# Performance work log

Hardware: AMD Instinct MI355X
Metric: run time of the kernel (lower is better)

## Reference

```python
import jax, jax.numpy as jnp
import numpy as np

B, L, D = 2, 4096, 128      # batch, seq_len, d_model
ED = 2 * D                  # d_inner (expand=2) = 256
N = 16                      # d_state
K = 4                       # d_conv
R = (D + 15) // 16          # dt_rank = 8
H = 2 * D                   # mlp hidden = 256


def setup_inputs() -> dict:
    key = jax.random.key(0)
    ks = jax.random.split(key, 20)
    s = 0.05
    inp = {
        "x": jax.random.normal(ks[0], (B, L, D), dtype=jnp.float32),
        # outer block LayerNorm (norm1)
        "norm1_g": jnp.ones((D,), jnp.float32),
        "norm1_b": jnp.zeros((D,), jnp.float32),
        # MambaLayer inner LayerNorm
        "inner_g": jnp.ones((D,), jnp.float32),
        "inner_b": jnp.zeros((D,), jnp.float32),
        # Mamba params
        "in_w": jax.random.normal(ks[1], (2 * ED, D), jnp.float32) * s,      # in_proj (no bias)
        "conv_w": jax.random.normal(ks[2], (ED, 1, K), jnp.float32) * s,     # depthwise conv
        "conv_b": jax.random.normal(ks[3], (ED,), jnp.float32) * s,
        "xproj_w": jax.random.normal(ks[4], (R + 2 * N, ED), jnp.float32) * s,  # x_proj (no bias)
        "dt_w": jax.random.normal(ks[5], (ED, R), jnp.float32) * s,
        "dt_b": jax.random.normal(ks[6], (ED,), jnp.float32) * s,
        "A_log": jnp.tile(jnp.log(jnp.arange(1, N + 1, dtype=jnp.float32)), (ED, 1)),  # [ED,N]
        "Dp": jnp.ones((ED,), jnp.float32),
        "out_w": jax.random.normal(ks[7], (D, ED), jnp.float32) * s,         # out_proj (no bias)
        # MLP
        "fc1_w": jax.random.normal(ks[8], (H, D), jnp.float32) * s,
        "fc1_b": jnp.zeros((H,), jnp.float32),
        "fc2_w": jax.random.normal(ks[9], (D, H), jnp.float32) * s,
        "fc2_b": jnp.zeros((D,), jnp.float32),
    }
    return inp


def _ln(x, g, b, eps=1e-5):
    m = jnp.mean(x, axis=-1, keepdims=True)
    v = jnp.mean((x - m) ** 2, axis=-1, keepdims=True)
    return (x - m) * jax.lax.rsqrt(v + eps) * g + b


def _mamba(x, in_w, conv_w, conv_b, xproj_w, dt_w, dt_b, A_log, Dp, out_w):
    # x: [B, L, D]
    xz = jnp.einsum('bld,ed->ble', x, in_w)          # [B,L,2*ED]
    u, z = jnp.split(xz, 2, axis=-1)                 # each [B,L,ED]
    # causal depthwise conv1d over L
    u_c = jnp.transpose(u, (0, 2, 1))                # [B,ED,L]
    u_c = jax.lax.conv_general_dilated(
        u_c, conv_w, window_strides=(1,), padding=[(K - 1, 0)],
        dimension_numbers=('NCH', 'OIH', 'NCH'), feature_group_count=ED)
    u = jax.nn.silu(jnp.transpose(u_c, (0, 2, 1)) + conv_b)   # [B,L,ED]
    # input-dependent dt, B, C
    dbc = jnp.einsum('ble,re->blr', u, xproj_w)      # [B,L,R+2N]
    dt, Bm, Cm = jnp.split(dbc, [R, R + N], axis=-1)
    delta = jax.nn.softplus(jnp.einsum('blr,er->ble', dt, dt_w) + dt_b)  # [B,L,ED]
    A = -jnp.exp(A_log)                              # [ED,N]
    deltaA = jnp.exp(jnp.einsum('ble,en->blen', delta, A))               # [B,L,ED,N]
    deltaBu = jnp.einsum('ble,bln,ble->blen', delta, Bm, u)              # [B,L,ED,N]
    # selective scan over L
    def step(h, inp):
        dA, dBu, Ct = inp                            # [B,ED,N],[B,ED,N],[B,N]
        h = dA * h + dBu
        y = jnp.einsum('ben,bn->be', h, Ct)
        return h, y
    h0 = jnp.zeros((B, ED, N), u.dtype)
    xs = (jnp.transpose(deltaA, (1, 0, 2, 3)),
          jnp.transpose(deltaBu, (1, 0, 2, 3)),
          jnp.transpose(Cm, (1, 0, 2)))
    _, ys = jax.lax.scan(step, h0, xs)               # [L,B,ED]
    y = jnp.transpose(ys, (1, 0, 2)) + u * Dp        # [B,L,ED]
    y = y * jax.nn.silu(z)
    return jnp.einsum('ble,de->bld', y, out_w)       # [B,L,D]


def reference(x, norm1_g, norm1_b, inner_g, inner_b, in_w, conv_w, conv_b,
              xproj_w, dt_w, dt_b, A_log, Dp, out_w, fc1_w, fc1_b, fc2_w, fc2_b):
    # attn branch: mamba(inner_LN(norm1(x)))
    a = _mamba(_ln(_ln(x, norm1_g, norm1_b), inner_g, inner_b),
               in_w, conv_w, conv_b, xproj_w, dt_w, dt_b, A_log, Dp, out_w)
    x = x + a
    # mlp branch (note: original applies norm1 again to updated x)
    h = _ln(x, norm1_g, norm1_b)
    h = jax.nn.gelu(jnp.einsum('bld,hd->blh', h, fc1_w) + fc1_b, approximate=False)
    h = jnp.einsum('blh,dh->bld', h, fc2_w) + fc2_b
    return x + h
```

## Files before the change

### kernel.cpp

```cpp
#include <hip/hip_runtime.h>
#include <hip/hip_bf16.h>
#include <math.h>

#define BB 2
#define LL 4096
#define DD 128
#define ED 256
#define NN 16
#define KK 4
#define RR 8
#define HH 256
#define NT (BB*LL)
#define NC 128
#define LC 32

#define LOG2E 1.4426950408889634f

typedef __attribute__((ext_vector_type(8))) short short8;
typedef __attribute__((ext_vector_type(8))) unsigned short ushort8v;
typedef __attribute__((ext_vector_type(4))) float floatx4;

__device__ __forceinline__ unsigned short f2bf(float f) {
  unsigned int b = __builtin_bit_cast(unsigned int, f);
  b += 0x7FFFu + ((b >> 16) & 1u);
  return (unsigned short)(b >> 16);
}

__device__ __forceinline__ float exp2_fast(float x) {
#if __has_builtin(__builtin_amdgcn_exp2f)
  return __builtin_amdgcn_exp2f(x);
#else
  return exp2f(x);
#endif
}

__device__ __forceinline__ ushort8v pack8(const float4& v0, const float4& v1) {
  ushort8v p;
  p[0]=f2bf(v0.x); p[1]=f2bf(v0.y); p[2]=f2bf(v0.z); p[3]=f2bf(v0.w);
  p[4]=f2bf(v1.x); p[5]=f2bf(v1.y); p[6]=f2bf(v1.z); p[7]=f2bf(v1.w);
  return p;
}

__global__ __launch_bounds__(256) void gemm_inln_k(const float* __restrict__ x,
    const float* __restrict__ g1, const float* __restrict__ b1,
    const float* __restrict__ g2, const float* __restrict__ b2,
    const float* __restrict__ W, float* __restrict__ C) {
  __shared__ unsigned short As[64][136];
  __shared__ unsigned short Ws[64][136];
  const int row0 = blockIdx.y * 64;
  const int col0 = blockIdx.x * 64;
  const int tid  = threadIdx.x;
  const int wave = tid >> 6, lane = tid & 63;
  const int quad = lane >> 4, l16 = lane & 15;
  const int wm = (wave & 1) * 32, wn = (wave >> 1) * 32;
  const int lr = tid >> 2;
  const int lk = (tid & 3) * 32;

  {
    const float* Ap = x + (size_t)(row0 + lr)*DD + lk;
    float4 av[8];
    float s = 0.f, sq = 0.f;
    #pragma unroll
    for (int g = 0; g < 8; g++) {
      av[g] = *(const float4*)(Ap + g*4);
      s  += av[g].x + av[g].y + av[g].z + av[g].w;
      sq += av[g].x*av[g].x + av[g].y*av[g].y + av[g].z*av[g].z + av[g].w*av[g].w;
    }
    s += __shfl_xor(s, 1);  s += __shfl_xor(s, 2);
    sq += __shfl_xor(sq, 1); sq += __shfl_xor(sq, 2);
    const float m1 = s * (1.f/128.f);
    const float rs1 = rsqrtf(sq*(1.f/128.f) - m1*m1 + 1e-5f);
    float s2 = 0.f, sq2 = 0.f;
    #pragma unroll
    for (int g = 0; g < 8; g++) {
      const float4 gg = *(const float4*)(g1 + lk + g*4);
      const float4 bb = *(const float4*)(b1 + lk + g*4);
      av[g].x = (av[g].x - m1)*rs1*gg.x + bb.x;
      av[g].y = (av[g].y - m1)*rs1*gg.y + bb.y;
      av[g].z = (av[g].z - m1)*rs1*gg.z + bb.z;
      av[g].w = (av[g].w - m1)*rs1*gg.w + bb.w;
      s2  += av[g].x + av[g].y + av[g].z + av[g].w;
      sq2 += av[g].x*av[g].x + av[g].y*av[g].y + av[g].z*av[g].z + av[g].w*av[g].w;
    }
    s2 += __shfl_xor(s2, 1);  s2 += __shfl_xor(s2, 2);
    sq2 += __shfl_xor(sq2, 1); sq2 += __shfl_xor(sq2, 2);
    const float m2 = s2 * (1.f/128.f);
    const float rs2 = rsqrtf(sq2*(1.f/128.f) - m2*m2 + 1e-5f);
    #pragma unroll
    for (int g = 0; g < 4; g++) {
      const float4 ga = *(const float4*)(g2 + lk + g*8);
      const float4 gb = *(const float4*)(g2 + lk + g*8 + 4);
      const float4 ba = *(const float4*)(b2 + lk + g*8);
      const float4 bbv= *(const float4*)(b2 + lk + g*8 + 4);
      ushort8v pa;
      pa[0] = f2bf((av[2*g].x   - m2)*rs2*ga.x + ba.x);
      pa[1] = f2bf((av[2*g].y   - m2)*rs2*ga.y + ba.y);
      pa[2] = f2bf((av[2*g].z   - m2)*rs2*ga.z + ba.z);
      pa[3] = f2bf((av[2*g].w   - m2)*rs2*ga.w + ba.w);
      pa[4] = f2bf((av[2*g+1].x - m2)*rs2*gb.x + bbv.x);
      pa[5] = f2bf((av[2*g+1].y - m2)*rs2*gb.y + bbv.y);
      pa[6] = f2bf((av[2*g+1].z - m2)*rs2*gb.z + bbv.z);
      pa[7] = f2bf((av[2*g+1].w - m2)*rs2*gb.w + bbv.w);
      *(ushort8v*)&As[lr][lk + g*8] = pa;
    }
  }
  {
    const float* Wp = W + (size_t)(col0 + lr)*DD + lk;
    #pragma unroll
    for (int g = 0; g < 4; g++) {
      const float4 v0 = *(const float4*)(Wp + g*8);
      const float4 v1 = *(const float4*)(Wp + g*8 + 4);
      *(ushort8v*)&Ws[lr][lk + g*8] = pack8(v0, v1);
    }
  }
  __syncthreads();

  floatx4 acc[2][2] = {};
  #pragma unroll
  for (int ks = 0; ks < 4; ks++) {
    const int ko = ks*32 + quad*8;
    short8 a0 = *(const short8*)&As[wm +      l16][ko];
    short8 a1 = *(const short8*)&As[wm + 16 + l16][ko];
    short8 b0 = *(const short8*)&Ws[wn +      l16][ko];
    short8 b1 = *(const short8*)&Ws[wn + 16 + l16][ko];
    acc[0][0] = __builtin_amdgcn_mfma_f32_16x16x32_bf16(a0, b0, acc[0][0], 0, 0, 0);
    acc[0][1] = __builtin_amdgcn_mfma_f32_16x16x32_bf16(a0, b1, acc[0][1], 0, 0, 0);
    acc[1][0] = __builtin_amdgcn_mfma_f32_16x16x32_bf16(a1, b0, acc[1][0], 0, 0, 0);
    acc[1][1] = __builtin_amdgcn_mfma_f32_16x16x32_bf16(a1, b1, acc[1][1], 0, 0, 0);
  }
  #pragma unroll
  for (int i = 0; i < 2; i++)
    #pragma unroll
    for (int j = 0; j < 2; j++) {
      const int n = col0 + wn + j*16 + l16;
      #pragma unroll
      for (int r = 0; r < 4; r++) {
        const int m = row0 + wm + i*16 + quad*4 + r;
        C[(size_t)m*(2*ED) + n] = acc[i][j][r];
      }
    }
}

__global__ __launch_bounds__(256) void scan1f_k(
    const float* __restrict__ xz, const float* __restrict__ cw,
    const float* __restrict__ cb, const float* __restrict__ xpw,
    const float* __restrict__ dtw, const float* __restrict__ dtb,
    const float* __restrict__ A_log, float* __restrict__ uc,
    float* __restrict__ dbc, float* __restrict__ delta,
    float* __restrict__ cA, float* __restrict__ cH) {
  __shared__ __align__(16) unsigned short Bs[64][264];
  __shared__ __align__(16) unsigned short As[32][264];
  __shared__ float su[32][128];
  __shared__ float sdbc[32][40];
  float (*sdel)[128] = reinterpret_cast<float(*)[128]>(&As[0][0]);

  const int eb = blockIdx.x, c = blockIdx.y, b = blockIdx.z;
  const int tid = threadIdx.x;
  const int t0 = b*LL + c*LC;

  #pragma unroll
  for (int p = 0; p < 8; p++) {
    const int idx = p*256 + tid;
    const int row = idx >> 5;
    const int col = (idx & 31) * 8;
    ushort8v v = {};
    if (row < 40) {
      const float4 v0 = *(const float4*)(xpw + (size_t)row*ED + col);
      const float4 v1 = *(const float4*)(xpw + (size_t)row*ED + col + 4);
      v = pack8(v0, v1);
    }
    *(ushort8v*)&Bs[row][col] = v;
  }

  {
    const int ch = tid;
    const float4 w = *(const float4*)(cw + ch*4);
    const float cbe = cb[ch];
    float xv[32];
    #pragma unroll
    for (int i = 0; i < LC; i++)
      xv[i] = xz[(size_t)(t0+i)*(2*ED) + ch];
    float h0 = 0.f, h1 = 0.f, h2 = 0.f;
    if (c != 0) {
      h0 = xz[(size_t)(t0-3)*(2*ED) + ch];
      h1 = xz[(size_t)(t0-2)*(2*ED) + ch];
      h2 = xz[(size_t)(t0-1)*(2*ED) + ch];
    }
    const bool own = (ch >> 7) == eb;
    #pragma unroll
    for (int i = 0; i < LC; i++) {
      const float cur = xv[i];
      const float a = cbe + h0*w.x + h1*w.y + h2*w.z + cur*w.w;
      const float s = a / (1.f + __expf(-a));
      As[i][ch] = f2bf(s);
      if (own) {
        su[i][ch & 127] = s;
        uc[(size_t)(t0+i)*ED + ch] = s;
      }
      h0 = h1; h1 = h2; h2 = cur;
    }
  }
  __syncthreads();

  const int wave = tid >> 6, lane = tid & 63;
  const int quad = lane >> 4, l16 = lane & 15;
  {
    const int mi = (wave & 1) * 16;
    const int j0 = (wave >> 1) * 2;
    floatx4 acc[2] = {};
    #pragma unroll
    for (int ks = 0; ks < 8; ks++) {
      const int ko = ks*32 + quad*8;
      short8 a  = *(const short8*)&As[mi + l16][ko];
      short8 b0 = *(const short8*)&Bs[j0*16 +      l16][ko];
      short8 b1 = *(const short8*)&Bs[j0*16 + 16 + l16][ko];
      acc[0] = __builtin_amdgcn_mfma_f32_16x16x32_bf16(a, b0, acc[0], 0, 0, 0);
      acc[1] = __builtin_amdgcn_mfma_f32_16x16x32_bf16(a, b1, acc[1], 0, 0, 0);
    }
    __syncthreads();
    #pragma unroll
    for (int f = 0; f < 2; f++) {
      const int n = (j0 + f)*16 + l16;
      #pragma unroll
      for (int r = 0; r < 4; r++) {
        const int m = mi + quad*4 + r;
        if (n < 40) {
          sdbc[m][n] = acc[f][r];
          if (eb == 0) dbc[(size_t)(t0 + m)*40 + n] = acc[f][r];
        }
      }
    }
  }
  __syncthreads();

  const int e_loc = tid >> 1;
  const int half  = tid & 1;
  const int e     = eb*128 + e_loc;
  {
    const float4 w0 = *(const float4*)(dtw + e*RR);
    const float4 w1 = *(const float4*)(dtw + e*RR + 4);
    const float db = dtb[e];
    #pragma unroll 4
    for (int i = 0; i < 16; i++) {
      const int t = half*16 + i;
      const float a = db
          + sdbc[t][0]*w0.x + sdbc[t][1]*w0.y + sdbc[t][2]*w0.z + sdbc[t][3]*w0.w
          + sdbc[t][4]*w1.x + sdbc[t][5]*w1.y + sdbc[t][6]*w1.z + sdbc[t][7]*w1.w;
      const float d = (a > 20.f) ? a : log1pf(__expf(a));
      sdel[t][e_loc] = d;
      delta[(size_t)(t0+t)*ED + e] = d;
    }
  }
  __syncthreads();

  const int n0 = half * 8;
  const float4 a0 = *(const float4*)(A_log + e*NN + n0);
  const float4 a1 = *(const float4*)(A_log + e*NN + n0 + 4);
  float Aen[8] = {-__expf(a0.x)*LOG2E, -__expf(a0.y)*LOG2E,
                  -__expf(a0.z)*LOG2E, -__expf(a0.w)*LOG2E,
                  -__expf(a1.x)*LOG2E, -__expf(a1.y)*LOG2E,
                  -__expf(a1.z)*LOG2E, -__expf(a1.w)*LOG2E};
  float h[8] = {};
  float sumd = 0.f;
  for (int i = 0; i < LC; i++) {
    const float dv = sdel[i][e_loc];
    const float du = dv * su[i][e_loc];
    const float4 B0 = *(const float4*)&sdbc[i][RR + n0];
    const float4 B1 = *(const float4*)&sdbc[i][RR + n0 + 4];
    const float Bv[8] = {B0.x,B0.y,B0.z,B0.w,B1.x,B1.y,B1.z,B1.w};
    sumd += dv;
    #pragma unroll
    for (int j = 0; j < 8; j++)
      h[j] = exp2_fast(dv * Aen[j])*h[j] + Bv[j]*du;
  }
  const size_t base = (((size_t)c*BB + b)*ED + e)*NN + n0;
  *(float4*)(cA + base)     = make_float4(exp2_fast(sumd*Aen[0]), exp2_fast(sumd*Aen[1]),
                                          exp2_fast(sumd*Aen[2]), exp2_fast(sumd*Aen[3]));
  *(float4*)(cA + base + 4) = make_float4(exp2_fast(sumd*Aen[4]), exp2_fast(sumd*Aen[5]),
                                          exp2_fast(sumd*Aen[6]), exp2_fast(sumd*Aen[7]));
  *(float4*)(cH + base)     = make_float4(h[0], h[1], h[2], h[3]);
  *(float4*)(cH + base + 4) = make_float4(h[4], h[5], h[6], h[7]);
}

__global__ __launch_bounds__(64) void scan2_k(float* __restrict__ cA,
    const float* __restrict__ cH) {
  const int gt = blockIdx.x*64 + threadIdx.x;
  const int b = gt >> 12;
  const size_t base = (size_t)b*ED*NN + (gt & 4095);
  float h = 0.f;
  for (int g = 0; g < NC/16; g++) {
    float av[16], hv[16];
    #pragma unroll
    for (int i = 0; i < 16; i++) {
      const size_t idx = (size_t)(g*16 + i)*(BB*ED*NN) + base;
      av[i] = cA[idx]; hv[i] = cH[idx];
    }
    #pragma unroll
    for (int i = 0; i < 16; i++) {
      const size_t idx = (size_t)(g*16 + i)*(BB*ED*NN) + base;
      cA[idx] = h;
      h = av[i]*h + hv[i];
    }
  }
}

__global__ __launch_bounds__(512, 1) void tail5_k(
    const float* __restrict__ xz, const float* __restrict__ delta,
    const float* __restrict__ uc, const float* __restrict__ dbc,
    const float* __restrict__ cP, const float* __restrict__ A_log,
    const float* __restrict__ Dpv, const float* __restrict__ x,
    const float* __restrict__ g1, const float* __restrict__ b1,
    const float* __restrict__ out_w, const float* __restrict__ fc1_w,
    const float* __restrict__ fc1_b, const float* __restrict__ fc2_w,
    const float* __restrict__ fc2_b, float* __restrict__ out) {
  __shared__ __align__(16) unsigned short BigW[34816];
  __shared__ __align__(16) unsigned short Au[32][264];
  __shared__ float xs[32][132];
  __shared__ float sbc[32][32];

  const int c = blockIdx.x, b = blockIdx.y;
  const int t0 = b*LL + c*LC;
  const int tid = threadIdx.x;
  const int wave = tid >> 6, lane = tid & 63;
  const int quad = lane >> 4, l16 = lane & 15;

  if (tid < 256) {
    const int row = tid >> 3, c4 = (tid & 7) * 4;
    *(float4*)&sbc[row][c4] = *(const float4*)(dbc + (size_t)(t0 + row)*40 + RR + c4);
  }
  __syncthreads();

  {
    const int r = tid >> 2, k0 = (tid & 3) * 64;
    const float* wp = out_w + (size_t)r*ED + k0;
    #pragma unroll
    for (int g = 0; g < 8; g++) {
      const float4 v0 = *(const float4*)(wp + g*8);
      const float4 v1 = *(const float4*)(wp + g*8 + 4);
      *(ushort8v*)&BigW[(size_t)r*264 + k0 + g*8] = pack8(v0, v1);
    }
  }

  {
    const int e = tid >> 1, half = tid & 1;
    const int n0 = half * 8;
    float Aen[8], h[8];
    {
      const float4 a0 = *(const float4*)(A_log + e*NN + n0);
      const float4 a1 = *(const float4*)(A_log + e*NN + n0 + 4);
      Aen[0]=-__expf(a0.x)*LOG2E; Aen[1]=-__expf(a0.y)*LOG2E;
      Aen[2]=-__expf(a0.z)*LOG2E; Aen[3]=-__expf(a0.w)*LOG2E;
      Aen[4]=-__expf(a1.x)*LOG2E; Aen[5]=-__expf(a1.y)*LOG2E;
      Aen[6]=-__expf(a1.z)*LOG2E; Aen[7]=-__expf(a1.w)*LOG2E;
      const size_t pb = (((size_t)c*BB + b)*ED + e)*NN + n0;
      const float4 h0 = *(const float4*)(cP + pb);
      const float4 h1 = *(const float4*)(cP + pb + 4);
      h[0]=h0.x; h[1]=h0.y; h[2]=h0.z; h[3]=h0.w;
      h[4]=h1.x; h[5]=h1.y; h[6]=h1.z; h[7]=h1.w;
    }
    const float Dpe = Dpv[e];
    float pd[8], pu[8], pz[8];
    #pragma unroll
    for (int i = 0; i < 8; i++) {
      pd[i] = delta[(size_t)(t0+i)*ED + e];
      pu[i] = uc[(size_t)(t0+i)*ED + e];
      pz[i] = xz[(size_t)(t0+i)*(2*ED) + ED + e];
    }
    for (int g4 = 0; g4 < 4; g4++) {
      float cd[8], cu[8], cz[8];
      #pragma unroll
      for (int i = 0; i < 8; i++) { cd[i]=pd[i]; cu[i]=pu[i]; cz[i]=pz[i]; }
      if (g4 < 3) {
        const int tn = t0 + (g4+1)*8;
        #pragma unroll
        for (int i = 0; i < 8; i++) {
          pd[i] = delta[(size_t)(tn+i)*ED + e];
          pu[i] = uc[(size_t)(tn+i)*ED + e];
          pz[i] = xz[(size_t)(tn+i)*(2*ED) + ED + e];
        }
      }
      #pragma unroll
      for (int i = 0; i < 8; i++) {
        const int t = g4*8 + i;
        const float dv = cd[i];
        const float uv = cu[i];
        const float du = dv * uv;
        const float4 B0 = *(const float4*)&sbc[t][n0];
        const float4 B1 = *(const float4*)&sbc[t][n0 + 4];
        const float4 C0 = *(const float4*)&sbc[t][16 + n0];
        const float4 C1 = *(const float4*)&sbc[t][16 + n0 + 4];
        const float Bv[8] = {B0.x,B0.y,B0.z,B0.w, B1.x,B1.y,B1.z,B1.w};
        const float Cv[8] = {C0.x,C0.y,C0.z,C0.w, C1.x,C1.y,C1.z,C1.w};
        float part = 0.f;
        #pragma unroll
        for (int j = 0; j < 8; j++) {
          h[j] = exp2_fast(dv * Aen[j])*h[j] + Bv[j]*du;
          part += h[j]*Cv[j];
        }
        part += __shfl_xor(part, 1);
        if (half == 0) {
          const float g = cz[i] / (1.f + __expf(-cz[i]));
          Au[t][e] = f2bf((part + uv*Dpe) * g);
        }
      }
    }
  }
  __syncthreads();

  {
    const int wn = wave * 16;
    floatx4 acc[2] = {};
    #pragma unroll
    for (int ks = 0; ks < 8; ks++) {
      const int ko = ks*32 + quad*8;
      short8 a0 = *(const short8*)&Au[l16][ko];
      short8 a1 = *(const short8*)&Au[16 + l16][ko];
      short8 bv = *(const short8*)&BigW[(size_t)(wn + l16)*264 + ko];
      acc[0] = __builtin_amdgcn_mfma_f32_16x16x32_bf16(a0, bv, acc[0], 0, 0, 0);
      acc[1] = __builtin_amdgcn_mfma_f32_16x16x32_bf16(a1, bv, acc[1], 0, 0, 0);
    }
    #pragma unroll
    for (int i = 0; i < 2; i++) {
      const int n = wn + l16;
      #pragma unroll
      for (int r = 0; r < 4; r++) {
        const int m = i*16 + quad*4 + r;
        xs[m][n] = acc[i][r] + x[(size_t)(t0 + m)*DD + n];
      }
    }
  }
  __syncthreads();

  {
    const int lr = tid >> 4, le = (tid & 15) * 8;
    float vv[8];
    float s = 0.f, sq = 0.f;
    #pragma unroll
    for (int i = 0; i < 8; i++) {
      vv[i] = xs[lr][le + i];
      s += vv[i]; sq += vv[i]*vv[i];
    }
    s += __shfl_xor(s, 1);  s += __shfl_xor(s, 2);
    s += __shfl_xor(s, 4);  s += __shfl_xor(s, 8);
    sq += __shfl_xor(sq, 1); sq += __shfl_xor(sq, 2);
    sq += __shfl_xor(sq, 4); sq += __shfl_xor(sq, 8);
    const float mean = s * (1.f/128.f);
    const float rs = rsqrtf(sq*(1.f/128.f) - mean*mean + 1e-5f);
    ushort8v p;
    #pragma unroll
    for (int i = 0; i < 8; i++)
      p[i] = f2bf((vv[i] - mean)*rs*g1[le + i] + b1[le + i]);
    *(ushort8v*)&Au[lr][le] = p;
  }
  {
    const int r = tid >> 1, k0 = (tid & 1) * 64;
    const float* wp = fc1_w + (size_t)r*DD + k0;
    #pragma unroll
    for (int g = 0; g < 8; g++) {
      const float4 v0 = *(const float4*)(wp + g*8);
      const float4 v1 = *(const float4*)(wp + g*8 + 4);
      *(ushort8v*)&BigW[(size_t)r*136 + k0 + g*8] = pack8(v0, v1);
    }
  }
  __syncthreads();

  {
    const int wn = wave * 32;
    floatx4 acc[2][2] = {};
    #pragma unroll
    for (int ks = 0; ks < 4; ks++) {
      const int ko = ks*32 + quad*8;
      short8 a0 = *(const short8*)&Au[l16][ko];
      short8 a1 = *(const short8*)&Au[16 + l16][ko];
      short8 b0 = *(const short8*)&BigW[(size_t)(wn +      l16)*136 + ko];
      short8 b1 = *(const short8*)&BigW[(size_t)(wn + 16 + l16)*136 + ko];
      acc[0][0] = __builtin_amdgcn_mfma_f32_16x16x32_bf16(a0, b0, acc[0][0], 0, 0, 0);
      acc[0][1] = __builtin_amdgcn_mfma_f32_16x16x32_bf16(a0, b1, acc[0][1], 0, 0, 0);
      acc[1][0] = __builtin_amdgcn_mfma_f32_16x16x32_bf16(a1, b0, acc[1][0], 0, 0, 0);
      acc[1][1] = __builtin_amdgcn_mfma_f32_16x16x32_bf16(a1, b1, acc[1][1], 0, 0, 0);
    }
    __syncthreads();
    #pragma unroll
    for (int i = 0; i < 2; i++)
      #pragma unroll
      for (int f = 0; f < 2; f++) {
        const int n = wn + f*16 + l16;
        const float bn = fc1_b[n];
        #pragma unroll
        for (int r = 0; r < 4; r++) {
          const int m = i*16 + quad*4 + r;
          float v = acc[i][f][r] + bn;
          v = 0.5f*v*(1.f + erff(v*0.70710678118f));
          Au[m][n] = f2bf(v);
        }
      }
  }
  {
    const int r = tid >> 2, k0 = (tid & 3) * 64;
    const float* wp = fc2_w + (size_t)r*HH + k0;
    __syncthreads();
    #pragma unroll
    for (int g = 0; g < 8; g++) {
      const float4 v0 = *(const float4*)(wp + g*8);
      const float4 v1 = *(const float4*)(wp + g*8 + 4);
      *(ushort8v*)&BigW[(size_t)r*264 + k0 + g*8] = pack8(v0, v1);
    }
  }
  __syncthreads();

  {
    const int wn = wave * 16;
    floatx4 acc[2] = {};
    #pragma unroll
    for (int ks = 0; ks < 8; ks++) {
      const int ko = ks*32 + quad*8;
      short8 a0 = *(const short8*)&Au[l16][ko];
      short8 a1 = *(const short8*)&Au[16 + l16][ko];
      short8 bv = *(const short8*)&BigW[(size_t)(wn + l16)*264 + ko];
      acc[0] = __builtin_amdgcn_mfma_f32_16x16x32_bf16(a0, bv, acc[0], 0, 0, 0);
      acc[1] = __builtin_amdgcn_mfma_f32_16x16x32_bf16(a1, bv, acc[1], 0, 0, 0);
    }
    #pragma unroll
    for (int i = 0; i < 2; i++) {
      const int n = wn + l16;
      const float bn = fc2_b[n];
      #pragma unroll
      for (int r = 0; r < 4; r++) {
        const int m = i*16 + quad*4 + r;
        out[(size_t)(t0 + m)*DD + n] = acc[i][r] + bn + xs[m][n];
      }
    }
  }
}

extern "C" void kernel_launch(void* const* d_in, const int* in_sizes, int n_in,
                              void* d_out, int out_size, void* d_ws, size_t ws_size,
                              hipStream_t stream) {
  const float* x      = (const float*)d_in[0];
  const float* n1g    = (const float*)d_in[1];
  const float* n1b    = (const float*)d_in[2];
  const float* ing    = (const float*)d_in[3];
  const float* inb    = (const float*)d_in[4];
  const float* in_w   = (const float*)d_in[5];
  const float* conv_w = (const float*)d_in[6];
  const float* conv_b = (const float*)d_in[7];
  const float* xproj_w= (const float*)d_in[8];
  const float* dt_w   = (const float*)d_in[9];
  const float* dt_b   = (const float*)d_in[10];
  const float* A_log  = (const float*)d_in[11];
  const float* Dpv    = (const float*)d_in[12];
  const float* out_w  = (const float*)d_in[13];
  const float* fc1_w  = (const float*)d_in[14];
  const float* fc1_b  = (const float*)d_in[15];
  const float* fc2_w  = (const float*)d_in[16];
  const float* fc2_b  = (const float*)d_in[17];
  float* out = (float*)d_out;

  float* ws    = (float*)d_ws;
  float* xz    = ws;
  float* uc    = xz    + (size_t)NT*2*ED;
  float* dbc   = uc    + (size_t)NT*ED;
  float* delta = dbc   + (size_t)NT*40;
  float* cAP   = delta + (size_t)NT*ED;
  float* cH    = cAP   + (size_t)NC*BB*ED*NN;

  gemm_inln_k<<<dim3(512/64, NT/64), 256, 0, stream>>>(x, n1g, n1b, ing, inb, in_w, xz);
  scan1f_k<<<dim3(2, NC, BB), 256, 0, stream>>>(xz, conv_w, conv_b, xproj_w, dt_w, dt_b,
                                                A_log, uc, dbc, delta, cAP, cH);
  scan2_k<<<(BB*ED*NN)/64, 64, 0, stream>>>(cAP, cH);
  tail5_k<<<dim3(NC, BB), 512, 0, stream>>>(xz, delta, uc, dbc, cAP, A_log, Dpv,
                                            x, n1g, n1b, out_w, fc1_w, fc1_b,
                                            fc2_w, fc2_b, out);
}
```

Measured before the change: 174.6 us.

## Fuse whole Mamba block into one cooperative kernel with grid sync

Replaces four separate launches (in_proj GEMM, chunk scan, cross-chunk scan, tail) with one cooperative kernel of 256 blocks. Each block recomputes its own in_proj chunk, including a 3-row halo for the conv, and keeps u, z, delta and B/C in a large LDS buffer instead of writing them to global memory. The cross-chunk state propagation presumably runs after a grid-wide sync. This removes the global round trips for xz, uc, delta and dbc plus the launch gaps. In exchange it uses about 150KB of LDS per block, which limits occupancy to one block per CU, and the halo rows are computed twice.

```diff
diff --git a/kernel.cpp b/kernel.cpp
--- a/kernel.cpp
+++ b/kernel.cpp
@@ -1,5 +1,5 @@
 #include <hip/hip_runtime.h>
-#include <hip/hip_bf16.h>
+#include <hip/hip_cooperative_groups.h>
 #include <math.h>
 
 #define BB 2
@@ -41,126 +41,43 @@
   return p;
 }
 
-__global__ __launch_bounds__(256) void gemm_inln_k(const float* __restrict__ x,
+__global__ __launch_bounds__(512, 2) void fused_k(
+    const float* __restrict__ x,
     const float* __restrict__ g1, const float* __restrict__ b1,
     const float* __restrict__ g2, const float* __restrict__ b2,
-    const float* __restrict__ W, float* __restrict__ C) {
-  __shared__ unsigned short As[64][136];
-  __shared__ unsigned short Ws[64][136];
-  const int row0 = blockIdx.y * 64;
-  const int col0 = blockIdx.x * 64;
-  const int tid  = threadIdx.x;
+    const float* __restrict__ in_w,
+    const float* __restrict__ cw, const float* __restrict__ cb,
+    const float* __restrict__ xpw,
+    const float* __restrict__ dtw, const float* __restrict__ dtb,
+    const float* __restrict__ A_log, const float* __restrict__ Dpv,
+    const float* __restrict__ out_w,
+    const float* __restrict__ fc1_w, const float* __restrict__ fc1_b,
+    const float* __restrict__ fc2_w, const float* __restrict__ fc2_b,
+    float* __restrict__ out, float* __restrict__ cA, float* __restrict__ cH) {
+  __shared__ __align__(16) unsigned char SM[154112];
+  float (*zs)[256]   = reinterpret_cast<float(*)[256]>(SM);
+  float (*sus)[256]  = reinterpret_cast<float(*)[256]>(SM + 32768);
+  float (*sdel)[256] = reinterpret_cast<float(*)[256]>(SM + 65536);
+  float (*sdbc)[40]  = reinterpret_cast<float(*)[40]>(SM + 98304);
+  unsigned short (*Bs)[264]    = reinterpret_cast<unsigned short(*)[264]>(SM + 103424);
+  unsigned short (*As)[264]    = reinterpret_cast<unsigned short(*)[264]>(SM + 137216);
+  unsigned short (*Au)[264]    = reinterpret_cast<unsigned short(*)[264]>(SM + 137216);
+  unsigned short (*Atile)[136] = reinterpret_cast<unsigned short(*)[136]>(SM + 137216);
+  unsigned short (*Wch)[136]   = reinterpret_cast<unsigned short(*)[136]>(SM + 32768);
+  float (*ubuf)[256] = reinterpret_cast<float(*)[256]>(SM + 67584);
+  float (*xsm)[132]  = reinterpret_cast<float(*)[132]>(SM);
+  unsigned short (*Wt)[264] = reinterpret_cast<unsigned short(*)[264]>(SM + 32768);
+  unsigned short (*W1)[136] = reinterpret_cast<unsigned short(*)[136]>(SM + 32768);
+
+  const int c = blockIdx.x, b = blockIdx.y;
+  const int t0 = b*LL + c*LC;
+  const int tid = threadIdx.x;
   const int wave = tid >> 6, lane = tid & 63;
   const int quad = lane >> 4, l16 = lane & 15;
-  const int wm = (wave & 1) * 32, wn = (wave >> 1) * 32;
-  const int lr = tid >> 2;
-  const int lk = (tid & 3) * 32;
-
-  {
-    const float* Ap = x + (size_t)(row0 + lr)*DD + lk;
-    float4 av[8];
-    float s = 0.f, sq = 0.f;
-    #pragma unroll
-    for (int g = 0; g < 8; g++) {
-      av[g] = *(const float4*)(Ap + g*4);
-      s  += av[g].x + av[g].y + av[g].z + av[g].w;
-      sq += av[g].x*av[g].x + av[g].y*av[g].y + av[g].z*av[g].z + av[g].w*av[g].w;
-    }
-    s += __shfl_xor(s, 1);  s += __shfl_xor(s, 2);
-    sq += __shfl_xor(sq, 1); sq += __shfl_xor(sq, 2);
-    const float m1 = s * (1.f/128.f);
-    const float rs1 = rsqrtf(sq*(1.f/128.f) - m1*m1 + 1e-5f);
-    float s2 = 0.f, sq2 = 0.f;
-    #pragma unroll
-    for (int g = 0; g < 8; g++) {
-      const float4 gg = *(const float4*)(g1 + lk + g*4);
-      const float4 bb = *(const float4*)(b1 + lk + g*4);
-      av[g].x = (av[g].x - m1)*rs1*gg.x + bb.x;
-      av[g].y = (av[g].y - m1)*rs1*gg.y + bb.y;
-      av[g].z = (av[g].z - m1)*rs1*gg.z + bb.z;
-      av[g].w = (av[g].w - m1)*rs1*gg.w + bb.w;
-      s2  += av[g].x + av[g].y + av[g].z + av[g].w;
-      sq2 += av[g].x*av[g].x + av[g].y*av[g].y + av[g].z*av[g].z + av[g].w*av[g].w;
-    }
-    s2 += __shfl_xor(s2, 1);  s2 += __shfl_xor(s2, 2);
-    sq2 += __shfl_xor(sq2, 1); sq2 += __shfl_xor(sq2, 2);
-    const float m2 = s2 * (1.f/128.f);
-    const float rs2 = rsqrtf(sq2*(1.f/128.f) - m2*m2 + 1e-5f);
-    #pragma unroll
-    for (int g = 0; g < 4; g++) {
-      const float4 ga = *(const float4*)(g2 + lk + g*8);
-      const float4 gb = *(const float4*)(g2 + lk + g*8 + 4);
-      const float4 ba = *(const float4*)(b2 + lk + g*8);
-      const float4 bbv= *(const float4*)(b2 + lk + g*8 + 4);
-      ushort8v pa;
-      pa[0] = f2bf((av[2*g].x   - m2)*rs2*ga.x + ba.x);
-      pa[1] = f2bf((av[2*g].y   - m2)*rs2*ga.y + ba.y);
-      pa[2] = f2bf((av[2*g].z   - m2)*rs2*ga.z + ba.z);
-      pa[3] = f2bf((av[2*g].w   - m2)*rs2*ga.w + ba.w);
-      pa[4] = f2bf((av[2*g+1].x - m2)*rs2*gb.x + bbv.x);
-      pa[5] = f2bf((av[2*g+1].y - m2)*rs2*gb.y + bbv.y);
-      pa[6] = f2bf((av[2*g+1].z - m2)*rs2*gb.z + bbv.z);
-      pa[7] = f2bf((av[2*g+1].w - m2)*rs2*gb.w + bbv.w);
-      *(ushort8v*)&As[lr][lk + g*8] = pa;
-    }
-  }
-  {
-    const float* Wp = W + (size_t)(col0 + lr)*DD + lk;
-    #pragma unroll
-    for (int g = 0; g < 4; g++) {
-      const float4 v0 = *(const float4*)(Wp + g*8);
-      const float4 v1 = *(const float4*)(Wp + g*8 + 4);
-      *(ushort8v*)&Ws[lr][lk + g*8] = pack8(v0, v1);
-    }
-  }
-  __syncthreads();
-
-  floatx4 acc[2][2] = {};
+
   #pragma unroll
-  for (int ks = 0; ks < 4; ks++) {
-    const int ko = ks*32 + quad*8;
-    short8 a0 = *(const short8*)&As[wm +      l16][ko];
-    short8 a1 = *(const short8*)&As[wm + 16 + l16][ko];
-    short8 b0 = *(const short8*)&Ws[wn +      l16][ko];
-    short8 b1 = *(const short8*)&Ws[wn + 16 + l16][ko];
-    acc[0][0] = __builtin_amdgcn_mfma_f32_16x16x32_bf16(a0, b0, acc[0][0], 0, 0, 0);
-    acc[0][1] = __builtin_amdgcn_mfma_f32_16x16x32_bf16(a0, b1, acc[0][1], 0, 0, 0);
-    acc[1][0] = __builtin_amdgcn_mfma_f32_16x16x32_bf16(a1, b0, acc[1][0], 0, 0, 0);
-    acc[1][1] = __builtin_amdgcn_mfma_f32_16x16x32_bf16(a1, b1, acc[1][1], 0, 0, 0);
-  }
-  #pragma unroll
-  for (int i = 0; i < 2; i++)
-    #pragma unroll
-    for (int j = 0; j < 2; j++) {
-      const int n = col0 + wn + j*16 + l16;
-      #pragma unroll
-      for (int r = 0; r < 4; r++) {
-        const int m = row0 + wm + i*16 + quad*4 + r;
-        C[(size_t)m*(2*ED) + n] = acc[i][j][r];
-      }
-    }
-}
-
-__global__ __launch_bounds__(256) void scan1f_k(
-    const float* __restrict__ xz, const float* __restrict__ cw,
-    const float* __restrict__ cb, const float* __restrict__ xpw,
-    const float* __restrict__ dtw, const float* __restrict__ dtb,
-    const float* __restrict__ A_log, float* __restrict__ uc,
-    float* __restrict__ dbc, float* __restrict__ delta,
-    float* __restrict__ cA, float* __restrict__ cH) {
-  __shared__ __align__(16) unsigned short Bs[64][264];
-  __shared__ __align__(16) unsigned short As[32][264];
-  __shared__ float su[32][128];
-  __shared__ float sdbc[32][40];
-  float (*sdel)[128] = reinterpret_cast<float(*)[128]>(&As[0][0]);
-
-  const int eb = blockIdx.x, c = blockIdx.y, b = blockIdx.z;
-  const int tid = threadIdx.x;
-  const int t0 = b*LL + c*LC;
-
-  #pragma unroll
-  for (int p = 0; p < 8; p++) {
-    const int idx = p*256 + tid;
+  for (int p = 0; p < 4; p++) {
+    const int idx = p*512 + tid;
     const int row = idx >> 5;
     const int col = (idx & 31) * 8;
     ushort8v v = {};
@@ -173,69 +90,146 @@
   }
 
   {
-    const int ch = tid;
+    const int lr = tid >> 2, lk = (tid & 3) * 32;
+    if (lr < 48) {
+      if (lr < 35 && !(c == 0 && lr < 3)) {
+        const float* Ap = x + (size_t)(t0 - 3 + lr)*DD + lk;
+        float4 av[8];
+        float s = 0.f, sq = 0.f;
+        #pragma unroll
+        for (int g = 0; g < 8; g++) {
+          av[g] = *(const float4*)(Ap + g*4);
+          s  += av[g].x + av[g].y + av[g].z + av[g].w;
+          sq += av[g].x*av[g].x + av[g].y*av[g].y + av[g].z*av[g].z + av[g].w*av[g].w;
+        }
+        s += __shfl_xor(s, 1);  s += __shfl_xor(s, 2);
+        sq += __shfl_xor(sq, 1); sq += __shfl_xor(sq, 2);
+        const float m1 = s * (1.f/128.f);
+        const float rs1 = rsqrtf(sq*(1.f/128.f) - m1*m1 + 1e-5f);
+        float s2 = 0.f, sq2 = 0.f;
+        #pragma unroll
+        for (int g = 0; g < 8; g++) {
+          const float4 gg = *(const float4*)(g1 + lk + g*4);
+          const float4 bb = *(const float4*)(b1 + lk + g*4);
+          av[g].x = (av[g].x - m1)*rs1*gg.x + bb.x;
+          av[g].y = (av[g].y - m1)*rs1*gg.y + bb.y;
+          av[g].z = (av[g].z - m1)*rs1*gg.z + bb.z;
+          av[g].w = (av[g].w - m1)*rs1*gg.w + bb.w;
+          s2  += av[g].x + av[g].y + av[g].z + av[g].w;
+          sq2 += av[g].x*av[g].x + av[g].y*av[g].y + av[g].z*av[g].z + av[g].w*av[g].w;
+        }
+        s2 += __shfl_xor(s2, 1);  s2 += __shfl_xor(s2, 2);
+        sq2 += __shfl_xor(sq2, 1); sq2 += __shfl_xor(sq2, 2);
+        const float m2 = s2 * (1.f/128.f);
+        const float rs2 = rsqrtf(sq2*(1.f/128.f) - m2*m2 + 1e-5f);
+        #pragma unroll
+        for (int g = 0; g < 4; g++) {
+          const float4 ga = *(const float4*)(g2 + lk + g*8);
+          const float4 gb = *(const float4*)(g2 + lk + g*8 + 4);
+          const float4 ba = *(const float4*)(b2 + lk + g*8);
+          const float4 bbv= *(const float4*)(b2 + lk + g*8 + 4);
+          ushort8v pa;
+          pa[0] = f2bf((av[2*g].x   - m2)*rs2*ga.x + ba.x);
+          pa[1] = f2bf((av[2*g].y   - m2)*rs2*ga.y + ba.y);
+          pa[2] = f2bf((av[2*g].z   - m2)*rs2*ga.z + ba.z);
+          pa[3] = f2bf((av[2*g].w   - m2)*rs2*ga.w + ba.w);
+          pa[4] = f2bf((av[2*g+1].x - m2)*rs2*gb.x + bbv.x);
+          pa[5] = f2bf((av[2*g+1].y - m2)*rs2*gb.y + bbv.y);
+          pa[6] = f2bf((av[2*g+1].z - m2)*rs2*gb.z + bbv.z);
+          pa[7] = f2bf((av[2*g+1].w - m2)*rs2*gb.w + bbv.w);
+          *(ushort8v*)&Atile[lr][lk + g*8] = pa;
+        }
+      } else {
+        const ushort8v zz = {};
+        #pragma unroll
+        for (int g = 0; g < 4; g++) *(ushort8v*)&Atile[lr][lk + g*8] = zz;
+      }
+    }
+  }
+  __syncthreads();
+
+  {
+    const int r = tid >> 2, seg = (tid & 3) * 32;
+    float4 wv[8];
+    #pragma unroll
+    for (int g = 0; g < 8; g++)
+      wv[g] = *(const float4*)(in_w + (size_t)r*DD + seg + g*4);
+    for (int wc = 0; wc < 4; wc++) {
+      #pragma unroll
+      for (int g = 0; g < 4; g++)
+        *(ushort8v*)&Wch[r][seg + g*8] = pack8(wv[2*g], wv[2*g+1]);
+      __syncthreads();
+      if (wc < 3) {
+        #pragma unroll
+        for (int g = 0; g < 8; g++)
+          wv[g] = *(const float4*)(in_w + (size_t)((wc+1)*128 + r)*DD + seg + g*4);
+      }
+      const int wn = wave * 16;
+      floatx4 acc[3] = {};
+      #pragma unroll
+      for (int ks = 0; ks < 4; ks++) {
+        const int ko = ks*32 + quad*8;
+        short8 bv = *(const short8*)&Wch[wn + l16][ko];
+        #pragma unroll
+        for (int mt = 0; mt < 3; mt++) {
+          short8 av = *(const short8*)&Atile[mt*16 + l16][ko];
+          acc[mt] = __builtin_amdgcn_mfma_f32_16x16x32_bf16(av, bv, acc[mt], 0, 0, 0);
+        }
+      }
+      const int ng = wc*128 + wn + l16;
+      #pragma unroll
+      for (int mt = 0; mt < 3; mt++)
+        #pragma unroll
+        for (int rr = 0; rr < 4; rr++) {
+          const int m = mt*16 + quad*4 + rr;
+          if (m < 35) {
+            if (ng < 256) ubuf[m][ng] = acc[mt][rr];
+            else if (m >= 3) zs[m-3][ng-256] = acc[mt][rr];
+          }
+        }
+      __syncthreads();
+    }
+  }
+
+  {
+    const int ch = tid & 255, th = tid >> 8;
+    const int i0 = th * 16;
     const float4 w = *(const float4*)(cw + ch*4);
     const float cbe = cb[ch];
-    float xv[32];
-    #pragma unroll
-    for (int i = 0; i < LC; i++)
-      xv[i] = xz[(size_t)(t0+i)*(2*ED) + ch];
-    float h0 = 0.f, h1 = 0.f, h2 = 0.f;
-    if (c != 0) {
-      h0 = xz[(size_t)(t0-3)*(2*ED) + ch];
-      h1 = xz[(size_t)(t0-2)*(2*ED) + ch];
-      h2 = xz[(size_t)(t0-1)*(2*ED) + ch];
-    }
-    const bool own = (ch >> 7) == eb;
-    #pragma unroll
-    for (int i = 0; i < LC; i++) {
-      const float cur = xv[i];
+    float h0 = ubuf[i0][ch], h1 = ubuf[i0+1][ch], h2 = ubuf[i0+2][ch];
+    #pragma unroll
+    for (int i = 0; i < 16; i++) {
+      const float cur = ubuf[i0+3+i][ch];
       const float a = cbe + h0*w.x + h1*w.y + h2*w.z + cur*w.w;
       const float s = a / (1.f + __expf(-a));
-      As[i][ch] = f2bf(s);
-      if (own) {
-        su[i][ch & 127] = s;
-        uc[(size_t)(t0+i)*ED + ch] = s;
-      }
+      As[i0+i][ch] = f2bf(s);
+      sus[i0+i][ch] = s;
       h0 = h1; h1 = h2; h2 = cur;
     }
   }
   __syncthreads();
 
-  const int wave = tid >> 6, lane = tid & 63;
-  const int quad = lane >> 4, l16 = lane & 15;
   {
     const int mi = (wave & 1) * 16;
-    const int j0 = (wave >> 1) * 2;
-    floatx4 acc[2] = {};
+    const int jn = (wave >> 1) * 16;
+    floatx4 acc = {};
     #pragma unroll
     for (int ks = 0; ks < 8; ks++) {
       const int ko = ks*32 + quad*8;
       short8 a  = *(const short8*)&As[mi + l16][ko];
-      short8 b0 = *(const short8*)&Bs[j0*16 +      l16][ko];
-      short8 b1 = *(const short8*)&Bs[j0*16 + 16 + l16][ko];
-      acc[0] = __builtin_amdgcn_mfma_f32_16x16x32_bf16(a, b0, acc[0], 0, 0, 0);
-      acc[1] = __builtin_amdgcn_mfma_f32_16x16x32_bf16(a, b1, acc[1], 0, 0, 0);
-    }
-    __syncthreads();
-    #pragma unroll
-    for (int f = 0; f < 2; f++) {
-      const int n = (j0 + f)*16 + l16;
-      #pragma unroll
-      for (int r = 0; r < 4; r++) {
-        const int m = mi + quad*4 + r;
-        if (n < 40) {
-          sdbc[m][n] = acc[f][r];
-          if (eb == 0) dbc[(size_t)(t0 + m)*40 + n] = acc[f][r];
-        }
-      }
-    }
-  }
-  __syncthreads();
-
-  const int e_loc = tid >> 1;
-  const int half  = tid & 1;
-  const int e     = eb*128 + e_loc;
+      short8 bv = *(const short8*)&Bs[jn + l16][ko];
+      acc = __builtin_amdgcn_mfma_f32_16x16x32_bf16(a, bv, acc, 0, 0, 0);
+    }
+    const int n = jn + l16;
+    if (n < 40) {
+      #pragma unroll
+      for (int rr = 0; rr < 4; rr++)
+        sdbc[mi + quad*4 + rr][n] = acc[rr];
+    }
+  }
+  __syncthreads();
+
+  const int e = tid >> 1, half = tid & 1;
   {
     const float4 w0 = *(const float4*)(dtw + e*RR);
     const float4 w1 = *(const float4*)(dtw + e*RR + 4);
@@ -247,86 +241,102 @@
           + sdbc[t][0]*w0.x + sdbc[t][1]*w0.y + sdbc[t][2]*w0.z + sdbc[t][3]*w0.w
           + sdbc[t][4]*w1.x + sdbc[t][5]*w1.y + sdbc[t][6]*w1.z + sdbc[t][7]*w1.w;
       const float d = (a > 20.f) ? a : log1pf(__expf(a));
-      sdel[t][e_loc] = d;
-      delta[(size_t)(t0+t)*ED + e] = d;
+      sdel[t][e] = d;
     }
   }
   __syncthreads();
 
   const int n0 = half * 8;
-  const float4 a0 = *(const float4*)(A_log + e*NN + n0);
-  const float4 a1 = *(const float4*)(A_log + e*NN + n0 + 4);
-  float Aen[8] = {-__expf(a0.x)*LOG2E, -__expf(a0.y)*LOG2E,
-                  -__expf(a0.z)*LOG2E, -__expf(a0.w)*LOG2E,
-                  -__expf(a1.x)*LOG2E, -__expf(a1.y)*LOG2E,
-                  -__expf(a1.z)*LOG2E, -__expf(a1.w)*LOG2E};
-  float h[8] = {};
-  float sumd = 0.f;
-  for (int i = 0; i < LC; i++) {
-    const float dv = sdel[i][e_loc];
-    const float du = dv * su[i][e_loc];
-    const float4 B0 = *(const float4*)&sdbc[i][RR + n0];
-    const float4 B1 = *(const float4*)&sdbc[i][RR + n0 + 4];
-    const float Bv[8] = {B0.x,B0.y,B0.z,B0.w,B1.x,B1.y,B1.z,B1.w};
-    sumd += dv;
-    #pragma unroll
-    for (int j = 0; j < 8; j++)
-      h[j] = exp2_fast(dv * Aen[j])*h[j] + Bv[j]*du;
-  }
-  const size_t base = (((size_t)c*BB + b)*ED + e)*NN + n0;
-  *(float4*)(cA + base)     = make_float4(exp2_fast(sumd*Aen[0]), exp2_fast(sumd*Aen[1]),
-                                          exp2_fast(sumd*Aen[2]), exp2_fast(sumd*Aen[3]));
-  *(float4*)(cA + base + 4) = make_float4(exp2_fast(sumd*Aen[4]), exp2_fast(sumd*Aen[5]),
-                                          exp2_fast(sumd*Aen[6]), exp2_fast(sumd*Aen[7]));
-  *(float4*)(cH + base)     = make_float4(h[0], h[1], h[2], h[3]);
-  *(float4*)(cH + base + 4) = make_float4(h[4], h[5], h[6], h[7]);
-}
-
-__global__ __launch_bounds__(64) void scan2_k(float* __restrict__ cA,
-    const float* __restrict__ cH) {
-  const int gt = blockIdx.x*64 + threadIdx.x;
-  const int b = gt >> 12;
-  const size_t base = (size_t)b*ED*NN + (gt & 4095);
-  float h = 0.f;
-  for (int g = 0; g < NC/16; g++) {
-    float av[16], hv[16];
-    #pragma unroll
-    for (int i = 0; i < 16; i++) {
-      const size_t idx = (size_t)(g*16 + i)*(BB*ED*NN) + base;
-      av[i] = cA[idx]; hv[i] = cH[idx];
-    }
-    #pragma unroll
-    for (int i = 0; i < 16; i++) {
-      const size_t idx = (size_t)(g*16 + i)*(BB*ED*NN) + base;
-      cA[idx] = h;
-      h = av[i]*h + hv[i];
-    }
-  }
-}
-
-__global__ __launch_bounds__(512, 1) void tail5_k(
-    const float* __restrict__ xz, const float* __restrict__ delta,
-    const float* __restrict__ uc, const float* __restrict__ dbc,
-    const float* __restrict__ cP, const float* __restrict__ A_log,
-    const float* __restrict__ Dpv, const float* __restrict__ x,
-    const float* __restrict__ g1, const float* __restrict__ b1,
-    const float* __restrict__ out_w, const float* __restrict__ fc1_w,
-    const float* __restrict__ fc1_b, const float* __restrict__ fc2_w,
-    const float* __restrict__ fc2_b, float* __restrict__ out) {
-  __shared__ __align__(16) unsigned short BigW[34816];
-  __shared__ __align__(16) unsigned short Au[32][264];
-  __shared__ float xs[32][132];
-  __shared__ float sbc[32][32];
-
-  const int c = blockIdx.x, b = blockIdx.y;
-  const int t0 = b*LL + c*LC;
-  const int tid = threadIdx.x;
-  const int wave = tid >> 6, lane = tid & 63;
-  const int quad = lane >> 4, l16 = lane & 15;
-
-  if (tid < 256) {
-    const int row = tid >> 3, c4 = (tid & 7) * 4;
-    *(float4*)&sbc[row][c4] = *(const float4*)(dbc + (size_t)(t0 + row)*40 + RR + c4);
+  float Aen[8];
+  {
+    const float4 a0 = *(const float4*)(A_log + e*NN + n0);
+    const float4 a1 = *(const float4*)(A_log + e*NN + n0 + 4);
+    Aen[0]=-__expf(a0.x)*LOG2E; Aen[1]=-__expf(a0.y)*LOG2E;
+    Aen[2]=-__expf(a0.z)*LOG2E; Aen[3]=-__expf(a0.w)*LOG2E;
+    Aen[4]=-__expf(a1.x)*LOG2E; Aen[5]=-__expf(a1.y)*LOG2E;
+    Aen[6]=-__expf(a1.z)*LOG2E; Aen[7]=-__expf(a1.w)*LOG2E;
+  }
+  {
+    float h[8] = {};
+    float sumd = 0.f;
+    for (int i = 0; i < LC; i++) {
+      const float dv = sdel[i][e];
+      const float du = dv * sus[i][e];
+      const float4 B0 = *(const float4*)&sdbc[i][RR + n0];
+      const float4 B1 = *(const float4*)&sdbc[i][RR + n0 + 4];
+      const float Bv[8] = {B0.x,B0.y,B0.z,B0.w,B1.x,B1.y,B1.z,B1.w};
+      sumd += dv;
+      #pragma unroll
+      for (int j = 0; j < 8; j++)
+        h[j] = exp2_fast(dv * Aen[j])*h[j] + Bv[j]*du;
+    }
+    const size_t base = (((size_t)c*BB + b)*ED + e)*NN + n0;
+    *(float4*)(cA + base)     = make_float4(exp2_fast(sumd*Aen[0]), exp2_fast(sumd*Aen[1]),
+                                            exp2_fast(sumd*Aen[2]), exp2_fast(sumd*Aen[3]));
+    *(float4*)(cA + base + 4) = make_float4(exp2_fast(sumd*Aen[4]), exp2_fast(sumd*Aen[5]),
+                                            exp2_fast(sumd*Aen[6]), exp2_fast(sumd*Aen[7]));
+    *(float4*)(cH + base)     = make_float4(h[0], h[1], h[2], h[3]);
+    *(float4*)(cH + base + 4) = make_float4(h[4], h[5], h[6], h[7]);
+  }
+  cooperative_groups::this_grid().sync();
+
+  {
+    const int bid = blockIdx.y * gridDim.x + blockIdx.x;
+    const int gt = bid*512 + tid;
+    if (gt < BB*ED*NN) {
+      const int bb = gt >> 12;
+      const size_t base = (size_t)bb*ED*NN + (gt & 4095);
+      float h = 0.f;
+      for (int g = 0; g < NC/16; g++) {
+        float av[16], hv[16];
+        #pragma unroll
+        for (int i = 0; i < 16; i++) {
+          const size_t idx = (size_t)(g*16 + i)*(BB*ED*NN) + base;
+          av[i] = cA[idx]; hv[i] = cH[idx];
+        }
+        #pragma unroll
+        for (int i = 0; i < 16; i++) {
+          const size_t idx = (size_t)(g*16 + i)*(BB*ED*NN) + base;
+          cA[idx] = h;
+          h = av[i]*h + hv[i];
+        }
+      }
+    }
+  }
+  cooperative_groups::this_grid().sync();
+
+  {
+    float h[8];
+    const size_t pb = (((size_t)c*BB + b)*ED + e)*NN + n0;
+    const float4 h0v = *(const float4*)(cA + pb);
+    const float4 h1v = *(const float4*)(cA + pb + 4);
+    h[0]=h0v.x; h[1]=h0v.y; h[2]=h0v.z; h[3]=h0v.w;
+    h[4]=h1v.x; h[5]=h1v.y; h[6]=h1v.z; h[7]=h1v.w;
+    const float Dpe = Dpv[e];
+    #pragma unroll 4
+    for (int t = 0; t < LC; t++) {
+      const float dv = sdel[t][e];
+      const float uv = sus[t][e];
+      const float du = dv * uv;
+      const float4 B0 = *(const float4*)&sdbc[t][RR + n0];
+      const float4 B1 = *(const float4*)&sdbc[t][RR + n0 + 4];
+      const float4 C0 = *(const float4*)&sdbc[t][RR + 16 + n0];
+      const float4 C1 = *(const float4*)&sdbc[t][RR + 16 + n0 + 4];
+      const float Bv[8] = {B0.x,B0.y,B0.z,B0.w, B1.x,B1.y,B1.z,B1.w};
+      const float Cv[8] = {C0.x,C0.y,C0.z,C0.w, C1.x,C1.y,C1.z,C1.w};
+      float part = 0.f;
+      #pragma unroll
+      for (int j = 0; j < 8; j++) {
+        h[j] = exp2_fast(dv * Aen[j])*h[j] + Bv[j]*du;
+        part += h[j]*Cv[j];
+      }
+      part += __shfl_xor(part, 1);
+      if (half == 0) {
+        const float zv = zs[t][e];
+        const float gv = zv / (1.f + __expf(-zv));
+        Au[t][e] = f2bf((part + uv*Dpe) * gv);
+      }
+    }
   }
   __syncthreads();
 
@@ -337,76 +347,10 @@
     for (int g = 0; g < 8; g++) {
       const float4 v0 = *(const float4*)(wp + g*8);
       const float4 v1 = *(const float4*)(wp + g*8 + 4);
-      *(ushort8v*)&BigW[(size_t)r*264 + k0 + g*8] = pack8(v0, v1);
-    }
-  }
-
-  {
-    const int e = tid >> 1, half = tid & 1;
-    const int n0 = half * 8;
-    float Aen[8], h[8];
-    {
-      const float4 a0 = *(const float4*)(A_log + e*NN + n0);
-      const float4 a1 = *(const float4*)(A_log + e*NN + n0 + 4);
-      Aen[0]=-__expf(a0.x)*LOG2E; Aen[1]=-__expf(a0.y)*LOG2E;
-      Aen[2]=-__expf(a0.z)*LOG2E; Aen[3]=-__expf(a0.w)*LOG2E;
-      Aen[4]=-__expf(a1.x)*LOG2E; Aen[5]=-__expf(a1.y)*LOG2E;
-      Aen[6]=-__expf(a1.z)*LOG2E; Aen[7]=-__expf(a1.w)*LOG2E;
-      const size_t pb = (((size_t)c*BB + b)*ED + e)*NN + n0;
-      const float4 h0 = *(const float4*)(cP + pb);
-      const float4 h1 = *(const float4*)(cP + pb + 4);
-      h[0]=h0.x; h[1]=h0.y; h[2]=h0.z; h[3]=h0.w;
-      h[4]=h1.x; h[5]=h1.y; h[6]=h1.z; h[7]=h1.w;
-    }
-    const float Dpe = Dpv[e];
-    float pd[8], pu[8], pz[8];
-    #pragma unroll
-    for (int i = 0; i < 8; i++) {
-      pd[i] = delta[(size_t)(t0+i)*ED + e];
-      pu[i] = uc[(size_t)(t0+i)*ED + e];
-      pz[i] = xz[(size_t)(t0+i)*(2*ED) + ED + e];
-    }
-    for (int g4 = 0; g4 < 4; g4++) {
-      float cd[8], cu[8], cz[8];
-      #pragma unroll
-      for (int i = 0; i < 8; i++) { cd[i]=pd[i]; cu[i]=pu[i]; cz[i]=pz[i]; }
-      if (g4 < 3) {
-        const int tn = t0 + (g4+1)*8;
-        #pragma unroll
-        for (int i = 0; i < 8; i++) {
-          pd[i] = delta[(size_t)(tn+i)*ED + e];
-          pu[i] = uc[(size_t)(tn+i)*ED + e];
-          pz[i] = xz[(size_t)(tn+i)*(2*ED) + ED + e];
-        }
-      }
-      #pragma unroll
-      for (int i = 0; i < 8; i++) {
-        const int t = g4*8 + i;
-        const float dv = cd[i];
-        const float uv = cu[i];
-        const float du = dv * uv;
-        const float4 B0 = *(const float4*)&sbc[t][n0];
-        const float4 B1 = *(const float4*)&sbc[t][n0 + 4];
-        const float4 C0 = *(const float4*)&sbc[t][16 + n0];
-        const float4 C1 = *(const float4*)&sbc[t][16 + n0 + 4];
-        const float Bv[8] = {B0.x,B0.y,B0.z,B0.w, B1.x,B1.y,B1.z,B1.w};
-        const float Cv[8] = {C0.x,C0.y,C0.z,C0.w, C1.x,C1.y,C1.z,C1.w};
-        float part = 0.f;
-        #pragma unroll
-        for (int j = 0; j < 8; j++) {
-          h[j] = exp2_fast(dv * Aen[j])*h[j] + Bv[j]*du;
-          part += h[j]*Cv[j];
-        }
-        part += __shfl_xor(part, 1);
-        if (half == 0) {
-          const float g = cz[i] / (1.f + __expf(-cz[i]));
-          Au[t][e] = f2bf((part + uv*Dpe) * g);
-        }
-      }
-    }
-  }
-  __syncthreads();
-
+      *(ushort8v*)&Wt[r][k0 + g*8] = pack8(v0, v1);
+    }
+  }
+  __syncthreads();
   {
     const int wn = wave * 16;
     floatx4 acc[2] = {};
@@ -415,7 +359,7 @@
       const int ko = ks*32 + quad*8;
       short8 a0 = *(const short8*)&Au[l16][ko];
       short8 a1 = *(const short8*)&Au[16 + l16][ko];
-      short8 bv = *(const short8*)&BigW[(size_t)(wn + l16)*264 + ko];
+      short8 bv = *(const short8*)&Wt[wn + l16][ko];
       acc[0] = __builtin_amdgcn_mfma_f32_16x16x32_bf16(a0, bv, acc[0], 0, 0, 0);
       acc[1] = __builtin_amdgcn_mfma_f32_16x16x32_bf16(a1, bv, acc[1], 0, 0, 0);
     }
@@ -423,9 +367,9 @@
     for (int i = 0; i < 2; i++) {
       const int n = wn + l16;
       #pragma unroll
-      for (int r = 0; r < 4; r++) {
-        const int m = i*16 + quad*4 + r;
-        xs[m][n] = acc[i][r] + x[(size_t)(t0 + m)*DD + n];
+      for (int rr = 0; rr < 4; rr++) {
+        const int m = i*16 + quad*4 + rr;
+        xsm[m][n] = acc[i][rr] + x[(size_t)(t0 + m)*DD + n];
       }
     }
   }
@@ -437,7 +381,7 @@
     float s = 0.f, sq = 0.f;
     #pragma unroll
     for (int i = 0; i < 8; i++) {
-      vv[i] = xs[lr][le + i];
+      vv[i] = xsm[lr][le + i];
       s += vv[i]; sq += vv[i]*vv[i];
     }
     s += __shfl_xor(s, 1);  s += __shfl_xor(s, 2);
@@ -459,7 +403,7 @@
     for (int g = 0; g < 8; g++) {
       const float4 v0 = *(const float4*)(wp + g*8);
       const float4 v1 = *(const float4*)(wp + g*8 + 4);
-      *(ushort8v*)&BigW[(size_t)r*136 + k0 + g*8] = pack8(v0, v1);
+      *(ushort8v*)&W1[r][k0 + g*8] = pack8(v0, v1);
     }
   }
   __syncthreads();
@@ -472,8 +416,8 @@
       const int ko = ks*32 + quad*8;
       short8 a0 = *(const short8*)&Au[l16][ko];
       short8 a1 = *(const short8*)&Au[16 + l16][ko];
-      short8 b0 = *(const short8*)&BigW[(size_t)(wn +      l16)*136 + ko];
-      short8 b1 = *(const short8*)&BigW[(size_t)(wn + 16 + l16)*136 + ko];
+      short8 b0 = *(const short8*)&W1[wn +      l16][ko];
+      short8 b1 = *(const short8*)&W1[wn + 16 + l16][ko];
       acc[0][0] = __builtin_amdgcn_mfma_f32_16x16x32_bf16(a0, b0, acc[0][0], 0, 0, 0);
       acc[0][1] = __builtin_amdgcn_mfma_f32_16x16x32_bf16(a0, b1, acc[0][1], 0, 0, 0);
       acc[1][0] = __builtin_amdgcn_mfma_f32_16x16x32_bf16(a1, b0, acc[1][0], 0, 0, 0);
@@ -487,9 +431,9 @@
         const int n = wn + f*16 + l16;
         const float bn = fc1_b[n];
         #pragma unroll
-        for (int r = 0; r < 4; r++) {
-          const int m = i*16 + quad*4 + r;
-          float v = acc[i][f][r] + bn;
+        for (int rr = 0; rr < 4; rr++) {
+          const int m = i*16 + quad*4 + rr;
+          float v = acc[i][f][rr] + bn;
           v = 0.5f*v*(1.f + erff(v*0.70710678118f));
           Au[m][n] = f2bf(v);
         }
@@ -498,12 +442,11 @@
   {
     const int r = tid >> 2, k0 = (tid & 3) * 64;
     const float* wp = fc2_w + (size_t)r*HH + k0;
-    __syncthreads();
     #pragma unroll
     for (int g = 0; g < 8; g++) {
       const float4 v0 = *(const float4*)(wp + g*8);
       const float4 v1 = *(const float4*)(wp + g*8 + 4);
-      *(ushort8v*)&BigW[(size_t)r*264 + k0 + g*8] = pack8(v0, v1);
+      *(ushort8v*)&Wt[r][k0 + g*8] = pack8(v0, v1);
     }
   }
   __syncthreads();
@@ -516,7 +459,7 @@
       const int ko = ks*32 + quad*8;
       short8 a0 = *(const short8*)&Au[l16][ko];
       short8 a1 = *(const short8*)&Au[16 + l16][ko];
-      short8 bv = *(const short8*)&BigW[(size_t)(wn + l16)*264 + ko];
+      short8 bv = *(const short8*)&Wt[wn + l16][ko];
       acc[0] = __builtin_amdgcn_mfma_f32_16x16x32_bf16(a0, bv, acc[0], 0, 0, 0);
       acc[1] = __builtin_amdgcn_mfma_f32_16x16x32_bf16(a1, bv, acc[1], 0, 0, 0);
     }
@@ -525,9 +468,9 @@
       const int n = wn + l16;
       const float bn = fc2_b[n];
       #pragma unroll
-      for (int r = 0; r < 4; r++) {
-        const int m = i*16 + quad*4 + r;
-        out[(size_t)(t0 + m)*DD + n] = acc[i][r] + bn + xs[m][n];
+      for (int rr = 0; rr < 4; rr++) {
+        const int m = i*16 + quad*4 + rr;
+        out[(size_t)(t0 + m)*DD + n] = acc[i][rr] + bn + xsm[m][n];
       }
     }
   }
@@ -556,19 +499,15 @@
   const float* fc2_b  = (const float*)d_in[17];
   float* out = (float*)d_out;
 
-  float* ws    = (float*)d_ws;
-  float* xz    = ws;
-  float* uc    = xz    + (size_t)NT*2*ED;
-  float* dbc   = uc    + (size_t)NT*ED;
-  float* delta = dbc   + (size_t)NT*40;
-  float* cAP   = delta + (size_t)NT*ED;
-  float* cH    = cAP   + (size_t)NC*BB*ED*NN;
-
-  gemm_inln_k<<<dim3(512/64, NT/64), 256, 0, stream>>>(x, n1g, n1b, ing, inb, in_w, xz);
-  scan1f_k<<<dim3(2, NC, BB), 256, 0, stream>>>(xz, conv_w, conv_b, xproj_w, dt_w, dt_b,
-                                                A_log, uc, dbc, delta, cAP, cH);
-  scan2_k<<<(BB*ED*NN)/64, 64, 0, stream>>>(cAP, cH);
-  tail5_k<<<dim3(NC, BB), 512, 0, stream>>>(xz, delta, uc, dbc, cAP, A_log, Dpv,
-                                            x, n1g, n1b, out_w, fc1_w, fc1_b,
-                                            fc2_w, fc2_b, out);
+  float* ws = (float*)d_ws;
+  float* cA = ws;
+  float* cH = cA + (size_t)NC*BB*ED*NN;
+
+  void* args[] = { (void*)&x, (void*)&n1g, (void*)&n1b, (void*)&ing, (void*)&inb,
+                   (void*)&in_w, (void*)&conv_w, (void*)&conv_b, (void*)&xproj_w,
+                   (void*)&dt_w, (void*)&dt_b, (void*)&A_log, (void*)&Dpv,
+                   (void*)&out_w, (void*)&fc1_w, (void*)&fc1_b, (void*)&fc2_w,
+                   (void*)&fc2_b, (void*)&out, (void*)&cA, (void*)&cH };
+  hipLaunchCooperativeKernel((const void*)fused_k, dim3(NC, BB), dim3(512),
+                             args, 0, stream);
 }
```

After: 242.6 us. 1.39x slower.
